# Optimization experiments

Hardware: AMD Instinct MI355X
Metric: run time of the kernel (lower is better)

The kernel has to match this reference:

```python
import jax, jax.numpy as jnp
import numpy as np

TEMPERATURE = 0.5
EPS = 1e-12  # matches torch F.normalize default eps


def _l2_normalize(x):
    norm = jnp.sqrt(jnp.sum(x * x, axis=-1, keepdims=True))
    return x / jnp.maximum(norm, EPS)


def setup_inputs() -> dict:
    key = jax.random.key(0)
    k1, k2 = jax.random.split(key)
    B, C, D = 64, 512, 256
    visual_features = jax.random.normal(k1, (B, C, D), dtype=jnp.float32)
    text_embeddings = jax.random.normal(k2, (B, C, D), dtype=jnp.float32)
    return {"visual_features": visual_features, "text_embeddings": text_embeddings}


def reference(visual_features, text_embeddings):
    v = _l2_normalize(visual_features)   # (B, C, D)
    t = _l2_normalize(text_embeddings)   # (B, C, D)
    # positive: diagonal similarity per class
    sim_pos = jnp.einsum('bcd,bcd->bc', v, t)
    positive = jnp.exp(sim_pos / TEMPERATURE)            # (B, C)
    # full BxCxC similarity matrix
    all_sim = jnp.exp(jnp.einsum('bcd,bkd->bck', v, t) / TEMPERATURE)
    negative = jnp.sum(all_sim, axis=-1) - positive      # (B, C)
    loss = -jnp.log(positive / (positive + negative))
    return jnp.mean(loss)
```

## Files before the change

kernel.cpp:

```cpp
#include <hip/hip_runtime.h>
#include <hip/hip_bf16.h>

#define BB 64
#define CC 512
#define DD 256

typedef __attribute__((ext_vector_type(8))) short bf16x8;
typedef __attribute__((ext_vector_type(4))) float f32x4;
typedef unsigned int u32;

#define SWZ(r) (((r) & 7) << 4)

__device__ inline short f2bf(float f) {
    union { __hip_bfloat16 h; short s; } cv;
    cv.h = __float2bfloat16(f);
    return cv.s;
}

__global__ __launch_bounds__(256) void norm_rows(const float* __restrict__ in,
                                                 unsigned short* __restrict__ out) {
    const int row  = blockIdx.x * 4 + (threadIdx.x >> 6);
    const int lane = threadIdx.x & 63;
    const float4 x = reinterpret_cast<const float4*>(in)[(size_t)row * 64 + lane];
    float ss = x.x * x.x + x.y * x.y + x.z * x.z + x.w * x.w;
#pragma unroll
    for (int off = 32; off; off >>= 1) ss += __shfl_xor(ss, off);
    const float r = 1.0f / fmaxf(sqrtf(ss), 1e-12f);
    ushort4 o;
    o.x = (unsigned short)f2bf(x.x * r);
    o.y = (unsigned short)f2bf(x.y * r);
    o.z = (unsigned short)f2bf(x.z * r);
    o.w = (unsigned short)f2bf(x.w * r);
    reinterpret_cast<ushort4*>(out)[(size_t)row * 64 + lane] = o;
}

__global__ __launch_bounds__(512, 1) void gemm_loss(const float* __restrict__ V,
                                                    const unsigned short* __restrict__ Tn,
                                                    float* __restrict__ partials) {
    extern __shared__ char lds[];
    float* vred = reinterpret_cast<float*>(lds + 131072);
    float* dred = vred + 256;
    float* red2 = dred + 256;

    const int i0    = blockIdx.x;
    const int inner = i0 & 63;
    const int b     = (inner & 7) * 8 + (inner >> 3);
    const int rb    = i0 >> 6;

    const int tid  = threadIdx.x;
    const int lane = tid & 63;
    const int wave = tid >> 6;
    const int wr   = wave >> 1;
    const int wc   = wave & 1;
    const int g    = lane >> 4;
    const int ln   = lane & 15;

    const float* gV = V + (size_t)b * (CC * DD) + (size_t)rb * 128 * DD;
    const char*  gT = reinterpret_cast<const char*>(Tn + (size_t)b * (CC * DD));

    {
        const int rrow  = tid >> 3;
        const int ecolB = (tid & 7) * 64;
#pragma unroll
        for (int p = 0; p < 2; ++p) {
            const int row = p * 64 + rrow;
            const float4* src =
                reinterpret_cast<const float4*>(gV + (size_t)row * DD) + (tid & 7) * 8;
            float4 x[8];
#pragma unroll
            for (int q = 0; q < 8; ++q) x[q] = src[q];
            float ss = 0.f;
#pragma unroll
            for (int q = 0; q < 8; ++q)
                ss += x[q].x * x[q].x + x[q].y * x[q].y + x[q].z * x[q].z + x[q].w * x[q].w;
            ss += __shfl_xor(ss, 1);
            ss += __shfl_xor(ss, 2);
            ss += __shfl_xor(ss, 4);
            const float rinv = 1.0f / fmaxf(sqrtf(ss), 1e-12f);
            char* dstrow = lds + row * 512;
            const int sw = SWZ(row);
#pragma unroll
            for (int q2 = 0; q2 < 4; ++q2) {
                const float4 v0 = x[2 * q2], v1 = x[2 * q2 + 1];
                bf16x8 o;
                o[0] = f2bf(v0.x * rinv); o[1] = f2bf(v0.y * rinv);
                o[2] = f2bf(v0.z * rinv); o[3] = f2bf(v0.w * rinv);
                o[4] = f2bf(v1.x * rinv); o[5] = f2bf(v1.y * rinv);
                o[6] = f2bf(v1.z * rinv); o[7] = f2bf(v1.w * rinv);
                *reinterpret_cast<bf16x8*>(dstrow + ((ecolB + q2 * 16) ^ sw)) = o;
            }
        }
    }
    __syncthreads();

    bf16x8 a[2][8];
#pragma unroll
    for (int i = 0; i < 2; ++i) {
        const int row  = wr * 32 + i * 16 + ln;
        const char* rp = lds + row * 512;
        const int sw   = SWZ(row);
#pragma unroll
        for (int kk = 0; kk < 8; ++kk)
            a[i][kk] = *reinterpret_cast<const bf16x8*>(rp + ((kk * 64 + g * 16) ^ sw));
    }
    __syncthreads();

    auto stage = [&](int t) {
        const char* gtile = gT + (size_t)t * 32768;
        char* dst = lds + (t & 3) * 32768 + wave * 4096;
#pragma unroll
        for (int r2 = 0; r2 < 4; ++r2) {
            const int L   = r2 * 1024 + (lane << 4);
            const int lr  = L >> 9;
            const int row = wave * 8 + lr;
            const int inrow = L & 511;
            __builtin_amdgcn_global_load_lds(
                (const u32*)(gtile + (size_t)row * 512 + (inrow ^ SWZ(row))),
                (u32*)(dst + r2 * 1024), 16, 0, 0);
        }
    };
    stage(0);
    stage(1);
    stage(2);

    float rs[2][4];
    float dg[2][4];
#pragma unroll
    for (int i = 0; i < 2; ++i)
#pragma unroll
        for (int r = 0; r < 4; ++r) { rs[i][r] = 0.f; dg[i][r] = 0.f; }

    for (int t = 0; t < 8; ++t) {
        if (t < 6)       asm volatile("s_waitcnt vmcnt(8)" ::: "memory");
        else if (t == 6) asm volatile("s_waitcnt vmcnt(4)" ::: "memory");
        else             asm volatile("s_waitcnt vmcnt(0)" ::: "memory");
        __builtin_amdgcn_s_barrier();
        __builtin_amdgcn_sched_barrier(0);
        if (t < 5) stage(t + 3);

        const char* bufp = lds + (t & 3) * 32768;
        const int row0 = wc * 32 + ln;
        const int row1 = wc * 32 + 16 + ln;
        const char* rp0 = bufp + row0 * 512;
        const char* rp1 = bufp + row1 * 512;
        const int sw0 = SWZ(row0), sw1 = SWZ(row1);
        f32x4 acc[2][2];
#pragma unroll
        for (int i = 0; i < 2; ++i)
#pragma unroll
            for (int j = 0; j < 2; ++j) acc[i][j] = (f32x4){0.f, 0.f, 0.f, 0.f};
        __builtin_amdgcn_s_setprio(1);
#pragma unroll
        for (int kk = 0; kk < 8; ++kk) {
            const int ko = kk * 64 + g * 16;
            const bf16x8 b0 = *reinterpret_cast<const bf16x8*>(rp0 + (ko ^ sw0));
            const bf16x8 b1 = *reinterpret_cast<const bf16x8*>(rp1 + (ko ^ sw1));
            acc[0][0] = __builtin_amdgcn_mfma_f32_16x16x32_bf16(a[0][kk], b0, acc[0][0], 0, 0, 0);
            acc[1][0] = __builtin_amdgcn_mfma_f32_16x16x32_bf16(a[1][kk], b0, acc[1][0], 0, 0, 0);
            acc[0][1] = __builtin_amdgcn_mfma_f32_16x16x32_bf16(a[0][kk], b1, acc[0][1], 0, 0, 0);
            acc[1][1] = __builtin_amdgcn_mfma_f32_16x16x32_bf16(a[1][kk], b1, acc[1][1], 0, 0, 0);
        }
        __builtin_amdgcn_s_setprio(0);

        if ((t >> 1) == rb) {
#pragma unroll
            for (int i = 0; i < 2; ++i) {
                const int grow = rb * 128 + wr * 32 + i * 16 + g * 4;
#pragma unroll
                for (int j = 0; j < 2; ++j) {
                    const int gcol = t * 64 + wc * 32 + j * 16 + ln;
#pragma unroll
                    for (int r = 0; r < 4; ++r) {
                        const float s2 = acc[i][j][r] * 2.0f;
                        rs[i][r] += __expf(s2);
                        if (gcol == grow + r) dg[i][r] += s2;
                    }
                }
            }
        } else {
#pragma unroll
            for (int i = 0; i < 2; ++i)
#pragma unroll
                for (int j = 0; j < 2; ++j)
#pragma unroll
                    for (int r = 0; r < 4; ++r) rs[i][r] += __expf(acc[i][j][r] * 2.0f);
        }
    }

#pragma unroll
    for (int i = 0; i < 2; ++i)
#pragma unroll
        for (int r = 0; r < 4; ++r) {
            float v = rs[i][r];
            float d = dg[i][r];
#pragma unroll
            for (int m = 1; m < 16; m <<= 1) {
                v += __shfl_xor(v, m);
                d += __shfl_xor(d, m);
            }
            if (ln == 0) {
                const int rl = wr * 32 + i * 16 + g * 4 + r;
                vred[rl * 2 + wc] = v;
                dred[rl * 2 + wc] = d;
            }
        }
    __syncthreads();

    if (tid < 128) {
        const float vv = vred[tid * 2] + vred[tid * 2 + 1];
        const float dd = dred[tid * 2] + dred[tid * 2 + 1];
        float lsum = logf(vv) - dd;
#pragma unroll
        for (int m = 1; m < 64; m <<= 1) lsum += __shfl_xor(lsum, m);
        if (lane == 0) red2[wave] = lsum;
    }
    __syncthreads();
    if (tid == 0) partials[i0] = red2[0] + red2[1];
}

__global__ __launch_bounds__(256) void final_reduce(const float* __restrict__ partials,
                                                    float* __restrict__ out) {
    const int t = threadIdx.x;
    float v = partials[t];
#pragma unroll
    for (int m = 1; m < 64; m <<= 1) v += __shfl_xor(v, m);
    __shared__ float red[4];
    if ((t & 63) == 0) red[t >> 6] = v;
    __syncthreads();
    if (t == 0) out[0] = (red[0] + red[1] + red[2] + red[3]) * (1.0f / 32768.0f);
}

extern "C" void kernel_launch(void* const* d_in, const int* in_sizes, int n_in,
                              void* d_out, int out_size, void* d_ws, size_t ws_size,
                              hipStream_t stream) {
    const float* vis = (const float*)d_in[0];
    const float* txt = (const float*)d_in[1];

    unsigned short* Tn = (unsigned short*)d_ws;
    float* partials    = (float*)((char*)d_ws + (size_t)BB * CC * DD * 2);
    float* out         = (float*)d_out;

    const int lds_bytes = 131072 + 256 * 4 + 256 * 4 + 16;
    hipFuncSetAttribute((const void*)gemm_loss, hipFuncAttributeMaxDynamicSharedMemorySize,
                        lds_bytes);

    norm_rows<<<8192, 256, 0, stream>>>(txt, Tn);
    gemm_loss<<<256, 512, lds_bytes, stream>>>(vis, Tn, partials);
    final_reduce<<<1, 256, 0, stream>>>(partials, out);
}
```

Baseline: 35.86 us.

## Fuse final reduction via last-block atomic counter and fold exp scale into norm

Removes the separate final_reduce launch: each gemm_loss block publishes its partial with a release store and bumps an atomic counter, and the last block sums all partials and writes the mean. Also folds the 2*log2(e) factor into the visual normalization so the inner loop uses a raw exp2 instead of a multiply plus __expf, rescaling the diagonal term by ln2. It adds a memset launch to reset the counter, and the bf16 rounding of the prescaled values changes numerics slightly.

```diff
diff --git a/kernel.cpp b/kernel.cpp
--- a/kernel.cpp
+++ b/kernel.cpp
@@ -10,6 +10,8 @@
 typedef unsigned int u32;
 
 #define SWZ(r) (((r) & 7) << 4)
+#define TWO_LOG2E 2.8853900817779268f
+#define LN2 0.6931471805599453f
 
 __device__ inline short f2bf(float f) {
     union { __hip_bfloat16 h; short s; } cv;
@@ -36,11 +38,15 @@
 
 __global__ __launch_bounds__(512, 1) void gemm_loss(const float* __restrict__ V,
                                                     const unsigned short* __restrict__ Tn,
-                                                    float* __restrict__ partials) {
+                                                    float* __restrict__ partials,
+                                                    unsigned* __restrict__ counter,
+                                                    float* __restrict__ out) {
     extern __shared__ char lds[];
     float* vred = reinterpret_cast<float*>(lds + 131072);
     float* dred = vred + 256;
     float* red2 = dred + 256;
+    __shared__ unsigned lastflag;
+    __shared__ float fr[8];
 
     const int i0    = blockIdx.x;
     const int inner = i0 & 63;
@@ -76,7 +82,7 @@
             ss += __shfl_xor(ss, 1);
             ss += __shfl_xor(ss, 2);
             ss += __shfl_xor(ss, 4);
-            const float rinv = 1.0f / fmaxf(sqrtf(ss), 1e-12f);
+            const float rinv = TWO_LOG2E / fmaxf(sqrtf(ss), 1e-12f);
             char* dstrow = lds + row * 512;
             const int sw = SWZ(row);
 #pragma unroll
@@ -171,9 +177,9 @@
                     const int gcol = t * 64 + wc * 32 + j * 16 + ln;
 #pragma unroll
                     for (int r = 0; r < 4; ++r) {
-                        const float s2 = acc[i][j][r] * 2.0f;
-                        rs[i][r] += __expf(s2);
-                        if (gcol == grow + r) dg[i][r] += s2;
+                        const float av = acc[i][j][r];
+                        rs[i][r] += __builtin_amdgcn_exp2f(av);
+                        if (gcol == grow + r) dg[i][r] += av * LN2;
                     }
                 }
             }
@@ -183,7 +189,8 @@
 #pragma unroll
                 for (int j = 0; j < 2; ++j)
 #pragma unroll
-                    for (int r = 0; r < 4; ++r) rs[i][r] += __expf(acc[i][j][r] * 2.0f);
+                    for (int r = 0; r < 4; ++r)
+                        rs[i][r] += __builtin_amdgcn_exp2f(acc[i][j][r]);
         }
     }
 
@@ -215,19 +222,30 @@
         if (lane == 0) red2[wave] = lsum;
     }
     __syncthreads();
-    if (tid == 0) partials[i0] = red2[0] + red2[1];
-}
-
-__global__ __launch_bounds__(256) void final_reduce(const float* __restrict__ partials,
-                                                    float* __restrict__ out) {
-    const int t = threadIdx.x;
-    float v = partials[t];
-#pragma unroll
-    for (int m = 1; m < 64; m <<= 1) v += __shfl_xor(v, m);
-    __shared__ float red[4];
-    if ((t & 63) == 0) red[t >> 6] = v;
-    __syncthreads();
-    if (t == 0) out[0] = (red[0] + red[1] + red[2] + red[3]) * (1.0f / 32768.0f);
+
+    if (tid == 0) {
+        __hip_atomic_store(&partials[i0], red2[0] + red2[1], __ATOMIC_RELEASE,
+                           __HIP_MEMORY_SCOPE_AGENT);
+        const unsigned prev =
+            __hip_atomic_fetch_add(counter, 1u, __ATOMIC_ACQ_REL, __HIP_MEMORY_SCOPE_AGENT);
+        lastflag = (prev == 255u) ? 1u : 0u;
+    }
+    __syncthreads();
+    if (lastflag) {
+        float v = 0.f;
+        if (tid < 256)
+            v = __hip_atomic_load(&partials[tid], __ATOMIC_ACQUIRE, __HIP_MEMORY_SCOPE_AGENT);
+#pragma unroll
+        for (int m = 1; m < 64; m <<= 1) v += __shfl_xor(v, m);
+        if (lane == 0) fr[wave] = v;
+        __syncthreads();
+        if (tid == 0) {
+            float s = 0.f;
+#pragma unroll
+            for (int w = 0; w < 8; ++w) s += fr[w];
+            out[0] = s * (1.0f / 32768.0f);
+        }
+    }
 }
 
 extern "C" void kernel_launch(void* const* d_in, const int* in_sizes, int n_in,
@@ -238,13 +256,14 @@
 
     unsigned short* Tn = (unsigned short*)d_ws;
     float* partials    = (float*)((char*)d_ws + (size_t)BB * CC * DD * 2);
+    unsigned* counter  = (unsigned*)(partials + 256);
     float* out         = (float*)d_out;
 
     const int lds_bytes = 131072 + 256 * 4 + 256 * 4 + 16;
     hipFuncSetAttribute((const void*)gemm_loss, hipFuncAttributeMaxDynamicSharedMemorySize,
                         lds_bytes);
 
+    hipMemsetAsync(counter, 0, sizeof(unsigned), stream);
     norm_rows<<<8192, 256, 0, stream>>>(txt, Tn);
-    gemm_loss<<<256, 512, lds_bytes, stream>>>(vis, Tn, partials);
-    final_reduce<<<1, 256, 0, stream>>>(partials, out);
-}
+    gemm_loss<<<256, 512, lds_bytes, stream>>>(vis, Tn, partials, counter, out);
+}
```

After: 70.18 us. 1.96x slower.
